# Optimization experiments

Measured on AMD Instinct MI355X. Metric: run time of the kernel, lower is better.

The kernel has to match this reference:

```python
import jax, jax.numpy as jnp
import numpy as np

N_NODES = 50000
N_EDGES = 800000
N_GRAPHS = 512
D = 128
NUM_LAYERS = 3
BN_EPS = 1e-5


def setup_inputs() -> dict:
    key = jax.random.key(0)
    ks = jax.random.split(key, 16)
    x = jax.random.normal(ks[0], (N_NODES, D), dtype=jnp.float32)
    edge_index = jax.random.randint(ks[1], (2, N_EDGES), 0, N_NODES, dtype=jnp.int64)
    batch = jnp.sort(jax.random.randint(ks[2], (N_NODES,), 0, N_GRAPHS, dtype=jnp.int64))
    # per-layer MLP params (all dims are 128 so we can stack across layers)
    s1 = 1.0 / np.sqrt(D)
    W1 = jax.random.uniform(ks[3], (NUM_LAYERS, D, D), jnp.float32, -s1, s1)
    b1 = jax.random.uniform(ks[4], (NUM_LAYERS, D), jnp.float32, -s1, s1)
    W2 = jax.random.uniform(ks[5], (NUM_LAYERS, D, D), jnp.float32, -s1, s1)
    b2 = jax.random.uniform(ks[6], (NUM_LAYERS, D), jnp.float32, -s1, s1)
    eps = jnp.zeros((NUM_LAYERS,), jnp.float32)  # train_eps=True, init 0.0
    gamma = jnp.ones((NUM_LAYERS, D), jnp.float32)
    beta = jnp.zeros((NUM_LAYERS, D), jnp.float32)
    return {"x": x, "edge_index": edge_index, "batch": batch,
            "W1": W1, "b1": b1, "W2": W2, "b2": b2,
            "eps": eps, "gamma": gamma, "beta": beta}


def _gin_forward(x, edge_index, batch, W1, b1, W2, b2, eps, gamma, beta):
    src, dst = edge_index[0], edge_index[1]
    h = x
    for i in range(NUM_LAYERS):
        # GINConv: MLP((1+eps)*h_i + sum_{j->i} h_j)  (scatter-add over edges)
        agg = jax.ops.segment_sum(h[src], dst, num_segments=N_NODES)
        z = (1.0 + eps[i]) * h + agg
        z = jax.nn.relu(z @ W1[i] + b1[i]) @ W2[i] + b2[i]
        # BatchNorm1d (training-mode batch stats, biased variance)
        mean = jnp.mean(z, axis=0)
        var = jnp.mean(jnp.square(z - mean), axis=0)
        h = (z - mean) * jax.lax.rsqrt(var + BN_EPS) * gamma[i] + beta[i]
        if i < NUM_LAYERS - 1:
            h = jax.nn.relu(h)  # dropout is identity in eval mode
    # global_mean_pool over batch segment ids
    sums = jax.ops.segment_sum(h, batch, num_segments=N_GRAPHS)
    counts = jax.ops.segment_sum(jnp.ones((N_NODES, 1), h.dtype), batch, num_segments=N_GRAPHS)
    return sums / jnp.maximum(counts, 1.0)


def reference(x, edge_index, batch, W1, b1, W2, b2, eps, gamma, beta):
    return _gin_forward(x, edge_index, batch, W1, b1, W2, b2, eps, gamma, beta)
```

## Files before the change

kernel.cpp:

```cpp
#include <hip/hip_runtime.h>

#define N_NODESC 50000
#define N_EDGESC 800000
#define N_GRAPHSC 512
#define DF 128
#define BN_EPSF 1e-5f
#define CSR_CAP 64
#define LAYER_BLOCKS 3125
#define NSLICE 32
#define POISON 0xAAAAAAAAu

#define PREP_SCAT_B 3125
#define PREP_CONVX_B 3125
#define PREP_CONVW_B 48
#define PREP_ZERO_B 6
#define PREP_TOTAL_B (PREP_SCAT_B + PREP_CONVX_B + PREP_CONVW_B + PREP_ZERO_B)

typedef _Float16 half8 __attribute__((ext_vector_type(8)));
typedef _Float16 half2v __attribute__((ext_vector_type(2)));
typedef float floatx4 __attribute__((ext_vector_type(4)));

__global__ __launch_bounds__(256) void k_prep(
    const int* __restrict__ src, const int* __restrict__ dst,
    unsigned* __restrict__ cursor, unsigned short* __restrict__ csr,
    const float* __restrict__ x, _Float16* __restrict__ h,
    const float* __restrict__ W1, const float* __restrict__ W2, half8* __restrict__ wf,
    float* __restrict__ pb2)
{
    int b = blockIdx.x;
    int tid = threadIdx.x;
    if (b < PREP_SCAT_B) {
        int e = b * 256 + tid;
        int d = dst[e];
        int sv = src[e];
        unsigned pos = atomicAdd(&cursor[d], 1u) - POISON;
        if (pos < CSR_CAP) csr[d * CSR_CAP + pos] = (unsigned short)sv;
    } else if (b < PREP_SCAT_B + PREP_CONVX_B) {
        int i8 = (b - PREP_SCAT_B) * 256 + tid;
        const floatx4* x4 = (const floatx4*)x;
        floatx4 v0 = __builtin_nontemporal_load(&x4[i8 * 2]);
        floatx4 v1 = __builtin_nontemporal_load(&x4[i8 * 2 + 1]);
        half8 o;
        o[0] = (_Float16)v0[0]; o[1] = (_Float16)v0[1]; o[2] = (_Float16)v0[2]; o[3] = (_Float16)v0[3];
        o[4] = (_Float16)v1[0]; o[5] = (_Float16)v1[1]; o[6] = (_Float16)v1[2]; o[7] = (_Float16)v1[3];
        ((half8*)h)[i8] = o;
    } else if (b < PREP_SCAT_B + PREP_CONVX_B + PREP_CONVW_B) {
        int t = (b - PREP_SCAT_B - PREP_CONVX_B) * 256 + tid;
        int m = t >> 11;
        int p = t & 2047;
        int ntile = p >> 8;
        int ks = (p >> 6) & 3;
        int l = p & 63;
        int n = ntile * 16 + (l & 15);
        int kb = ks * 32 + (l >> 4) * 8;
        const float* W = (m < 3) ? (W1 + (size_t)m * DF * DF) : (W2 + (size_t)(m - 3) * DF * DF);
        half8 o;
#pragma unroll
        for (int j = 0; j < 8; j++) o[j] = (_Float16)W[(size_t)(kb + j) * DF + n];
        wf[t] = o;
    } else {
        int b2 = b - (PREP_SCAT_B + PREP_CONVX_B + PREP_CONVW_B);
        floatx4* p4 = (floatx4*)pb2;
        int base = (b2 * 256 + tid) * 4;
#pragma unroll
        for (int j = 0; j < 4; j++) p4[base + j] = (floatx4)(0.f);
    }
}

#define TSTRIDE 136
template <int MODE>
__global__ __launch_bounds__(1024) void k_layer(
    const _Float16* __restrict__ Hin, const unsigned* __restrict__ cursor,
    const unsigned short* __restrict__ csr,
    const float* __restrict__ epsArr, int layer,
    const float* __restrict__ pbPrev, const float* __restrict__ gprev, const float* __restrict__ bprev,
    const half8* __restrict__ W1f, const float* __restrict__ b1,
    const half8* __restrict__ W2f, const float* __restrict__ b2,
    _Float16* __restrict__ Z, float* __restrict__ pbOut)
{
    __shared__ _Float16 At[16 * TSTRIDE];
    __shared__ _Float16 Bt[16 * TSTRIDE];
    __shared__ float red[4][256];
    __shared__ float scof[DF], ofof[DF];
    const int tid = threadIdx.x;
    const int w = tid >> 6, lane = tid & 63;

    if (MODE == 1) {
        int cc = tid & 255, sg = tid >> 8;
        float s = 0.f;
#pragma unroll
        for (int sl = 0; sl < 8; sl++) s += pbPrev[(sg + sl * 4) * 256 + cc];
        red[sg][cc] = s;
        __syncthreads();
        if (tid < 128) {
            const float invN = 1.f / (float)N_NODESC;
            float su = red[0][tid] + red[1][tid] + red[2][tid] + red[3][tid];
            float sq = red[0][128 + tid] + red[1][128 + tid] + red[2][128 + tid] + red[3][128 + tid];
            float m = su * invN;
            float var = sq * invN - m * m;
            float sc = gprev[tid] * rsqrtf(var + BN_EPSF);
            scof[tid] = sc;
            ofof[tid] = bprev[tid] - m * sc;
        }
        __syncthreads();
    }

    {
        int n = blockIdx.x * 16 + w;
        int g = lane >> 4, c16 = lane & 15;
        float sc[8], of[8];
        if (MODE == 1) {
#pragma unroll
            for (int i = 0; i < 8; i++) {
                sc[i] = scof[c16 * 8 + i];
                of[i] = ofof[c16 * 8 + i];
            }
        }
        const half8* Hr8 = (const half8*)Hin;
        int myidx = (int)csr[n * CSR_CAP + lane];
        int deg = (int)(cursor[n] - POISON);
        if (deg > CSR_CAP) deg = CSR_CAP;

        float a[8];
#pragma unroll
        for (int i = 0; i < 8; i++) a[i] = 0.f;
        if (g == 0) {
            half8 u = Hr8[(size_t)n * 16 + c16];
            float e1 = 1.0f + epsArr[layer];
#pragma unroll
            for (int i = 0; i < 8; i++) {
                float xv = (float)u[i];
                if (MODE == 1) xv = fmaxf(xv * sc[i] + of[i], 0.f);
                a[i] = e1 * xv;
            }
        }
        int T = (deg + 7) >> 3;
        int k = g;
        for (int t = 0; t < T; t++, k += 8) {
            int m0 = __shfl(myidx, k);
            int m1 = __shfl(myidx, k + 4);
            bool ok0 = k < deg, ok1 = (k + 4) < deg;
            int mm0 = ok0 ? m0 : n;
            int mm1 = ok1 ? m1 : n;
            half8 u0 = Hr8[(size_t)mm0 * 16 + c16];
            half8 u1 = Hr8[(size_t)mm1 * 16 + c16];
            float f0 = ok0 ? 1.f : 0.f, f1 = ok1 ? 1.f : 0.f;
#pragma unroll
            for (int i = 0; i < 8; i++) {
                float x0 = (float)u0[i], x1 = (float)u1[i];
                if (MODE == 1) {
                    x0 = fmaxf(x0 * sc[i] + of[i], 0.f);
                    x1 = fmaxf(x1 * sc[i] + of[i], 0.f);
                }
                a[i] = fmaf(f0, x0, a[i]);
                a[i] = fmaf(f1, x1, a[i]);
            }
        }
#pragma unroll
        for (int i = 0; i < 8; i++) {
            a[i] += __shfl_xor(a[i], 16);
            a[i] += __shfl_xor(a[i], 32);
        }
        if (g == 0) {
            half8 o;
#pragma unroll
            for (int i = 0; i < 8; i++) o[i] = (_Float16)a[i];
            *(half8*)&At[w * TSTRIDE + c16 * 8] = o;
        }
    }
    __syncthreads();

    const int q = lane >> 4, c = lane & 15;
    if (w < 8) {
        half8 af[4];
#pragma unroll
        for (int ks = 0; ks < 4; ks++)
            af[ks] = *(const half8*)&At[c * TSTRIDE + ks * 32 + q * 8];
        floatx4 acc = (floatx4)(0.0f);
#pragma unroll
        for (int ks = 0; ks < 4; ks++) {
            half8 wfr = W1f[(w * 4 + ks) * 64 + lane];
            acc = __builtin_amdgcn_mfma_f32_16x16x32_f16(af[ks], wfr, acc, 0, 0, 0);
        }
        float b = b1[w * 16 + c];
#pragma unroll
        for (int r = 0; r < 4; r++) {
            float vv = fmaxf(acc[r] + b, 0.f);
            Bt[(q * 4 + r) * TSTRIDE + w * 16 + c] = (_Float16)vv;
        }
    }
    __syncthreads();

    if (w < 8) {
        half8 bf[4];
#pragma unroll
        for (int ks = 0; ks < 4; ks++)
            bf[ks] = *(const half8*)&Bt[c * TSTRIDE + ks * 32 + q * 8];
        floatx4 acc2 = (floatx4)(0.0f);
#pragma unroll
        for (int ks = 0; ks < 4; ks++) {
            half8 wfr = W2f[(w * 4 + ks) * 64 + lane];
            acc2 = __builtin_amdgcn_mfma_f32_16x16x32_f16(bf[ks], wfr, acc2, 0, 0, 0);
        }
        float b = b2[w * 16 + c];
        float ls = 0.f, lq = 0.f;
#pragma unroll
        for (int r = 0; r < 4; r++) {
            float vv = acc2[r] + b;
            ls += vv;
            lq += vv * vv;
            At[(q * 4 + r) * TSTRIDE + w * 16 + c] = (_Float16)vv;
        }
        ls += __shfl_xor(ls, 16);
        ls += __shfl_xor(ls, 32);
        lq += __shfl_xor(lq, 16);
        lq += __shfl_xor(lq, 32);
        if (q == 0) {
            float* pbb = pbOut + (size_t)(blockIdx.x & (NSLICE - 1)) * 256;
            atomicAdd(&pbb[w * 16 + c], ls);
            atomicAdd(&pbb[128 + w * 16 + c], lq);
        }
    }
    __syncthreads();

    half2v vz = *(const half2v*)&At[w * TSTRIDE + 2 * lane];
    ((half2v*)Z)[(size_t)(blockIdx.x * 16 + w) * 64 + lane] = vz;
}

static __device__ int lbound(const int* __restrict__ a, int n, int key) {
    int lo = 0, hi = n;
    while (lo < hi) {
        int mid = (lo + hi) >> 1;
        if (a[mid] < key) lo = mid + 1; else hi = mid;
    }
    return lo;
}

__global__ __launch_bounds__(128) void k_pool(const _Float16* __restrict__ Z, const int* __restrict__ batch,
                                              const float* __restrict__ pbL2, const float* __restrict__ gamma,
                                              const float* __restrict__ beta, float* __restrict__ out) {
    __shared__ int bnds[2];
    int g = blockIdx.x, c = threadIdx.x;
    if (threadIdx.x == 0) {
        bnds[0] = lbound(batch, N_NODESC, g);
        bnds[1] = lbound(batch, N_NODESC, g + 1);
    }
    float su = 0.f, sq = 0.f;
#pragma unroll 8
    for (int sl = 0; sl < NSLICE; sl++) {
        su += pbL2[sl * 256 + c];
        sq += pbL2[sl * 256 + 128 + c];
    }
    __syncthreads();
    const float invN = 1.f / (float)N_NODESC;
    float m = su * invN;
    float v = sq * invN - m * m;
    float sc = gamma[c] * rsqrtf(v + BN_EPSF);
    float of = beta[c] - m * sc;
    int lo = bnds[0], hi = bnds[1];
    float s = 0.f;
    int r = lo;
    for (; r + 4 <= hi; r += 4) {
        s += (float)Z[(size_t)r * DF + c] + (float)Z[(size_t)(r + 1) * DF + c]
           + (float)Z[(size_t)(r + 2) * DF + c] + (float)Z[(size_t)(r + 3) * DF + c];
    }
    for (; r < hi; r++) s += (float)Z[(size_t)r * DF + c];
    int cnt = hi - lo;
    out[g * DF + c] = (cnt > 0) ? (s / (float)cnt) * sc + of : 0.f;
}

extern "C" void kernel_launch(void* const* d_in, const int* in_sizes, int n_in,
                              void* d_out, int out_size, void* d_ws, size_t ws_size,
                              hipStream_t stream) {
    const float* x     = (const float*)d_in[0];
    const int*   ei    = (const int*)d_in[1];
    const int*   batch = (const int*)d_in[2];
    const float* W1    = (const float*)d_in[3];
    const float* b1    = (const float*)d_in[4];
    const float* W2    = (const float*)d_in[5];
    const float* b2    = (const float*)d_in[6];
    const float* eps   = (const float*)d_in[7];
    const float* gamma = (const float*)d_in[8];
    const float* beta  = (const float*)d_in[9];
    float* out = (float*)d_out;

    char* ws = (char*)d_ws;
    size_t o = 0;
    auto alloc = [&](size_t bytes) -> char* {
        char* p = ws + o;
        o += (bytes + 255) & ~(size_t)255;
        return p;
    };
    unsigned* cursor = (unsigned*)alloc(N_NODESC * sizeof(unsigned));
    unsigned short* csr = (unsigned short*)alloc((size_t)N_NODESC * CSR_CAP * sizeof(unsigned short));
    float* pb2     = (float*)alloc((size_t)3 * NSLICE * 256 * sizeof(float));
    half8* wf      = (half8*)alloc((size_t)6 * 2048 * sizeof(half8));
    _Float16* hbuf = (_Float16*)alloc((size_t)N_NODESC * DF * sizeof(_Float16));
    _Float16* za   = (_Float16*)alloc((size_t)N_NODESC * DF * sizeof(_Float16));
    _Float16* zb   = (_Float16*)alloc((size_t)N_NODESC * DF * sizeof(_Float16));
    (void)ws_size; (void)in_sizes; (void)n_in; (void)out_size;

    const int* srcA = ei;
    const int* dstA = ei + N_EDGESC;

    k_prep<<<PREP_TOTAL_B, 256, 0, stream>>>(srcA, dstA, cursor, csr, x, hbuf, W1, W2, wf, pb2);

    k_layer<0><<<LAYER_BLOCKS, 1024, 0, stream>>>(
        hbuf, cursor, csr, eps, 0, nullptr, nullptr, nullptr,
        wf + 0 * 2048, b1 + 0 * DF, wf + 3 * 2048, b2 + 0 * DF, za, pb2 + 0 * 8192);
    k_layer<1><<<LAYER_BLOCKS, 1024, 0, stream>>>(
        za, cursor, csr, eps, 1, pb2 + 0 * 8192, gamma + 0 * DF, beta + 0 * DF,
        wf + 1 * 2048, b1 + 1 * DF, wf + 4 * 2048, b2 + 1 * DF, zb, pb2 + 1 * 8192);
    k_layer<1><<<LAYER_BLOCKS, 1024, 0, stream>>>(
        zb, cursor, csr, eps, 2, pb2 + 1 * 8192, gamma + 1 * DF, beta + 1 * DF,
        wf + 2 * 2048, b1 + 2 * DF, wf + 5 * 2048, b2 + 2 * DF, za, pb2 + 2 * 8192);
    k_pool<<<N_GRAPHSC, DF, 0, stream>>>(za, batch, pb2 + 2 * 8192, gamma + 2 * DF, beta + 2 * DF, out);
}
```

Measured before the change: 272.6 us.

## Fuse prep, three GIN layers and pooling into one cooperative persistent kernel

Replaces the five separate launches (prep, three layer kernels, pool) with a single cooperative kernel that strides over tiles and uses grid-wide syncs between phases. It aims to remove launch gaps and the tail of each kernel. In exchange the grid is capped at about two 1024-thread blocks per CU. Each grid.sync costs a global barrier, and the launch_bounds hint may raise register pressure and lower occupancy for the gather-bound layer work.

```diff
diff --git a/kernel.cpp b/kernel.cpp
--- a/kernel.cpp
+++ b/kernel.cpp
@@ -1,4 +1,7 @@
 #include <hip/hip_runtime.h>
+#include <hip/hip_cooperative_groups.h>
+
+namespace cg = cooperative_groups;
 
 #define N_NODESC 50000
 #define N_EDGESC 800000
@@ -14,218 +17,11 @@
 #define PREP_CONVX_B 3125
 #define PREP_CONVW_B 48
 #define PREP_ZERO_B 6
-#define PREP_TOTAL_B (PREP_SCAT_B + PREP_CONVX_B + PREP_CONVW_B + PREP_ZERO_B)
+#define PREP_UNITS (PREP_SCAT_B + PREP_CONVX_B + PREP_CONVW_B + PREP_ZERO_B)
 
 typedef _Float16 half8 __attribute__((ext_vector_type(8)));
 typedef _Float16 half2v __attribute__((ext_vector_type(2)));
 typedef float floatx4 __attribute__((ext_vector_type(4)));
-
-__global__ __launch_bounds__(256) void k_prep(
-    const int* __restrict__ src, const int* __restrict__ dst,
-    unsigned* __restrict__ cursor, unsigned short* __restrict__ csr,
-    const float* __restrict__ x, _Float16* __restrict__ h,
-    const float* __restrict__ W1, const float* __restrict__ W2, half8* __restrict__ wf,
-    float* __restrict__ pb2)
-{
-    int b = blockIdx.x;
-    int tid = threadIdx.x;
-    if (b < PREP_SCAT_B) {
-        int e = b * 256 + tid;
-        int d = dst[e];
-        int sv = src[e];
-        unsigned pos = atomicAdd(&cursor[d], 1u) - POISON;
-        if (pos < CSR_CAP) csr[d * CSR_CAP + pos] = (unsigned short)sv;
-    } else if (b < PREP_SCAT_B + PREP_CONVX_B) {
-        int i8 = (b - PREP_SCAT_B) * 256 + tid;
-        const floatx4* x4 = (const floatx4*)x;
-        floatx4 v0 = __builtin_nontemporal_load(&x4[i8 * 2]);
-        floatx4 v1 = __builtin_nontemporal_load(&x4[i8 * 2 + 1]);
-        half8 o;
-        o[0] = (_Float16)v0[0]; o[1] = (_Float16)v0[1]; o[2] = (_Float16)v0[2]; o[3] = (_Float16)v0[3];
-        o[4] = (_Float16)v1[0]; o[5] = (_Float16)v1[1]; o[6] = (_Float16)v1[2]; o[7] = (_Float16)v1[3];
-        ((half8*)h)[i8] = o;
-    } else if (b < PREP_SCAT_B + PREP_CONVX_B + PREP_CONVW_B) {
-        int t = (b - PREP_SCAT_B - PREP_CONVX_B) * 256 + tid;
-        int m = t >> 11;
-        int p = t & 2047;
-        int ntile = p >> 8;
-        int ks = (p >> 6) & 3;
-        int l = p & 63;
-        int n = ntile * 16 + (l & 15);
-        int kb = ks * 32 + (l >> 4) * 8;
-        const float* W = (m < 3) ? (W1 + (size_t)m * DF * DF) : (W2 + (size_t)(m - 3) * DF * DF);
-        half8 o;
-#pragma unroll
-        for (int j = 0; j < 8; j++) o[j] = (_Float16)W[(size_t)(kb + j) * DF + n];
-        wf[t] = o;
-    } else {
-        int b2 = b - (PREP_SCAT_B + PREP_CONVX_B + PREP_CONVW_B);
-        floatx4* p4 = (floatx4*)pb2;
-        int base = (b2 * 256 + tid) * 4;
-#pragma unroll
-        for (int j = 0; j < 4; j++) p4[base + j] = (floatx4)(0.f);
-    }
-}
-
-#define TSTRIDE 136
-template <int MODE>
-__global__ __launch_bounds__(1024) void k_layer(
-    const _Float16* __restrict__ Hin, const unsigned* __restrict__ cursor,
-    const unsigned short* __restrict__ csr,
-    const float* __restrict__ epsArr, int layer,
-    const float* __restrict__ pbPrev, const float* __restrict__ gprev, const float* __restrict__ bprev,
-    const half8* __restrict__ W1f, const float* __restrict__ b1,
-    const half8* __restrict__ W2f, const float* __restrict__ b2,
-    _Float16* __restrict__ Z, float* __restrict__ pbOut)
-{
-    __shared__ _Float16 At[16 * TSTRIDE];
-    __shared__ _Float16 Bt[16 * TSTRIDE];
-    __shared__ float red[4][256];
-    __shared__ float scof[DF], ofof[DF];
-    const int tid = threadIdx.x;
-    const int w = tid >> 6, lane = tid & 63;
-
-    if (MODE == 1) {
-        int cc = tid & 255, sg = tid >> 8;
-        float s = 0.f;
-#pragma unroll
-        for (int sl = 0; sl < 8; sl++) s += pbPrev[(sg + sl * 4) * 256 + cc];
-        red[sg][cc] = s;
-        __syncthreads();
-        if (tid < 128) {
-            const float invN = 1.f / (float)N_NODESC;
-            float su = red[0][tid] + red[1][tid] + red[2][tid] + red[3][tid];
-            float sq = red[0][128 + tid] + red[1][128 + tid] + red[2][128 + tid] + red[3][128 + tid];
-            float m = su * invN;
-            float var = sq * invN - m * m;
-            float sc = gprev[tid] * rsqrtf(var + BN_EPSF);
-            scof[tid] = sc;
-            ofof[tid] = bprev[tid] - m * sc;
-        }
-        __syncthreads();
-    }
-
-    {
-        int n = blockIdx.x * 16 + w;
-        int g = lane >> 4, c16 = lane & 15;
-        float sc[8], of[8];
-        if (MODE == 1) {
-#pragma unroll
-            for (int i = 0; i < 8; i++) {
-                sc[i] = scof[c16 * 8 + i];
-                of[i] = ofof[c16 * 8 + i];
-            }
-        }
-        const half8* Hr8 = (const half8*)Hin;
-        int myidx = (int)csr[n * CSR_CAP + lane];
-        int deg = (int)(cursor[n] - POISON);
-        if (deg > CSR_CAP) deg = CSR_CAP;
-
-        float a[8];
-#pragma unroll
-        for (int i = 0; i < 8; i++) a[i] = 0.f;
-        if (g == 0) {
-            half8 u = Hr8[(size_t)n * 16 + c16];
-            float e1 = 1.0f + epsArr[layer];
-#pragma unroll
-            for (int i = 0; i < 8; i++) {
-                float xv = (float)u[i];
-                if (MODE == 1) xv = fmaxf(xv * sc[i] + of[i], 0.f);
-                a[i] = e1 * xv;
-            }
-        }
-        int T = (deg + 7) >> 3;
-        int k = g;
-        for (int t = 0; t < T; t++, k += 8) {
-            int m0 = __shfl(myidx, k);
-            int m1 = __shfl(myidx, k + 4);
-            bool ok0 = k < deg, ok1 = (k + 4) < deg;
-            int mm0 = ok0 ? m0 : n;
-            int mm1 = ok1 ? m1 : n;
-            half8 u0 = Hr8[(size_t)mm0 * 16 + c16];
-            half8 u1 = Hr8[(size_t)mm1 * 16 + c16];
-            float f0 = ok0 ? 1.f : 0.f, f1 = ok1 ? 1.f : 0.f;
-#pragma unroll
-            for (int i = 0; i < 8; i++) {
-                float x0 = (float)u0[i], x1 = (float)u1[i];
-                if (MODE == 1) {
-                    x0 = fmaxf(x0 * sc[i] + of[i], 0.f);
-                    x1 = fmaxf(x1 * sc[i] + of[i], 0.f);
-                }
-                a[i] = fmaf(f0, x0, a[i]);
-                a[i] = fmaf(f1, x1, a[i]);
-            }
-        }
-#pragma unroll
-        for (int i = 0; i < 8; i++) {
-            a[i] += __shfl_xor(a[i], 16);
-            a[i] += __shfl_xor(a[i], 32);
-        }
-        if (g == 0) {
-            half8 o;
-#pragma unroll
-            for (int i = 0; i < 8; i++) o[i] = (_Float16)a[i];
-            *(half8*)&At[w * TSTRIDE + c16 * 8] = o;
-        }
-    }
-    __syncthreads();
-
-    const int q = lane >> 4, c = lane & 15;
-    if (w < 8) {
-        half8 af[4];
-#pragma unroll
-        for (int ks = 0; ks < 4; ks++)
-            af[ks] = *(const half8*)&At[c * TSTRIDE + ks * 32 + q * 8];
-        floatx4 acc = (floatx4)(0.0f);
-#pragma unroll
-        for (int ks = 0; ks < 4; ks++) {
-            half8 wfr = W1f[(w * 4 + ks) * 64 + lane];
-            acc = __builtin_amdgcn_mfma_f32_16x16x32_f16(af[ks], wfr, acc, 0, 0, 0);
-        }
-        float b = b1[w * 16 + c];
-#pragma unroll
-        for (int r = 0; r < 4; r++) {
-            float vv = fmaxf(acc[r] + b, 0.f);
-            Bt[(q * 4 + r) * TSTRIDE + w * 16 + c] = (_Float16)vv;
-        }
-    }
-    __syncthreads();
-
-    if (w < 8) {
-        half8 bf[4];
-#pragma unroll
-        for (int ks = 0; ks < 4; ks++)
-            bf[ks] = *(const half8*)&Bt[c * TSTRIDE + ks * 32 + q * 8];
-        floatx4 acc2 = (floatx4)(0.0f);
-#pragma unroll
-        for (int ks = 0; ks < 4; ks++) {
-            half8 wfr = W2f[(w * 4 + ks) * 64 + lane];
-            acc2 = __builtin_amdgcn_mfma_f32_16x16x32_f16(bf[ks], wfr, acc2, 0, 0, 0);
-        }
-        float b = b2[w * 16 + c];
-        float ls = 0.f, lq = 0.f;
-#pragma unroll
-        for (int r = 0; r < 4; r++) {
-            float vv = acc2[r] + b;
-            ls += vv;
-            lq += vv * vv;
-            At[(q * 4 + r) * TSTRIDE + w * 16 + c] = (_Float16)vv;
-        }
-        ls += __shfl_xor(ls, 16);
-        ls += __shfl_xor(ls, 32);
-        lq += __shfl_xor(lq, 16);
-        lq += __shfl_xor(lq, 32);
-        if (q == 0) {
-            float* pbb = pbOut + (size_t)(blockIdx.x & (NSLICE - 1)) * 256;
-            atomicAdd(&pbb[w * 16 + c], ls);
-            atomicAdd(&pbb[128 + w * 16 + c], lq);
-        }
-    }
-    __syncthreads();
-
-    half2v vz = *(const half2v*)&At[w * TSTRIDE + 2 * lane];
-    ((half2v*)Z)[(size_t)(blockIdx.x * 16 + w) * 64 + lane] = vz;
-}
 
 static __device__ int lbound(const int* __restrict__ a, int n, int key) {
     int lo = 0, hi = n;
@@ -236,37 +32,265 @@
     return lo;
 }
 
-__global__ __launch_bounds__(128) void k_pool(const _Float16* __restrict__ Z, const int* __restrict__ batch,
-                                              const float* __restrict__ pbL2, const float* __restrict__ gamma,
-                                              const float* __restrict__ beta, float* __restrict__ out) {
-    __shared__ int bnds[2];
-    int g = blockIdx.x, c = threadIdx.x;
-    if (threadIdx.x == 0) {
-        bnds[0] = lbound(batch, N_NODESC, g);
-        bnds[1] = lbound(batch, N_NODESC, g + 1);
+#define TSTRIDE 136
+
+__global__ __launch_bounds__(1024, 8) void k_all(
+    const int* __restrict__ src, const int* __restrict__ dst,
+    unsigned* __restrict__ cursor, unsigned short* __restrict__ csr,
+    const float* __restrict__ x, _Float16* __restrict__ hbuf,
+    const float* __restrict__ W1, const float* __restrict__ b1,
+    const float* __restrict__ W2, const float* __restrict__ b2,
+    half8* __restrict__ wf, float* __restrict__ pb2,
+    const float* __restrict__ epsArr, const float* __restrict__ gamma, const float* __restrict__ beta,
+    const int* __restrict__ batch, _Float16* __restrict__ za, _Float16* __restrict__ zb,
+    float* __restrict__ out)
+{
+    cg::grid_group grid = cg::this_grid();
+    const int tid = threadIdx.x;
+    const int nb = gridDim.x;
+
+    __shared__ _Float16 At[16 * TSTRIDE];
+    __shared__ _Float16 Bt[16 * TSTRIDE];
+    __shared__ float red[4][256];
+    __shared__ float scof[DF], ofof[DF];
+    __shared__ int bnds2[8][2];
+
+    for (int F = blockIdx.x * 1024 + tid; F < PREP_UNITS * 256; F += nb * 1024) {
+        int b = F >> 8;
+        int t2 = F & 255;
+        if (b < PREP_SCAT_B) {
+            int e = F;
+            int d = dst[e];
+            int sv = src[e];
+            unsigned pos = atomicAdd(&cursor[d], 1u) - POISON;
+            if (pos < CSR_CAP) csr[d * CSR_CAP + pos] = (unsigned short)sv;
+        } else if (b < PREP_SCAT_B + PREP_CONVX_B) {
+            int i8 = (b - PREP_SCAT_B) * 256 + t2;
+            const floatx4* x4 = (const floatx4*)x;
+            floatx4 v0 = __builtin_nontemporal_load(&x4[i8 * 2]);
+            floatx4 v1 = __builtin_nontemporal_load(&x4[i8 * 2 + 1]);
+            half8 o;
+            o[0] = (_Float16)v0[0]; o[1] = (_Float16)v0[1]; o[2] = (_Float16)v0[2]; o[3] = (_Float16)v0[3];
+            o[4] = (_Float16)v1[0]; o[5] = (_Float16)v1[1]; o[6] = (_Float16)v1[2]; o[7] = (_Float16)v1[3];
+            ((half8*)hbuf)[i8] = o;
+        } else if (b < PREP_SCAT_B + PREP_CONVX_B + PREP_CONVW_B) {
+            int t = (b - PREP_SCAT_B - PREP_CONVX_B) * 256 + t2;
+            int m = t >> 11;
+            int p = t & 2047;
+            int ntile = p >> 8;
+            int ks = (p >> 6) & 3;
+            int l = p & 63;
+            int n = ntile * 16 + (l & 15);
+            int kb = ks * 32 + (l >> 4) * 8;
+            const float* W = (m < 3) ? (W1 + (size_t)m * DF * DF) : (W2 + (size_t)(m - 3) * DF * DF);
+            half8 o;
+#pragma unroll
+            for (int j = 0; j < 8; j++) o[j] = (_Float16)W[(size_t)(kb + j) * DF + n];
+            wf[t] = o;
+        } else {
+            int b2 = b - (PREP_SCAT_B + PREP_CONVX_B + PREP_CONVW_B);
+            floatx4* p4 = (floatx4*)pb2;
+            int base = (b2 * 256 + t2) * 4;
+#pragma unroll
+            for (int j = 0; j < 4; j++) p4[base + j] = (floatx4)(0.f);
+        }
     }
-    float su = 0.f, sq = 0.f;
+    grid.sync();
+
+    const int w = tid >> 6, lane = tid & 63;
+    const int q = lane >> 4, c = lane & 15;
+
+    for (int l = 0; l < 3; l++) {
+        const _Float16* Hin = (l == 0) ? hbuf : ((l == 1) ? za : zb);
+        _Float16* Z = (l == 1) ? zb : za;
+        const half8* W1f = wf + (size_t)l * 2048;
+        const half8* W2f = wf + (size_t)(3 + l) * 2048;
+        const float* bb1 = b1 + l * DF;
+        const float* bb2 = b2 + l * DF;
+        float* pbOut = pb2 + (size_t)l * 8192;
+
+        if (l > 0) {
+            const float* pbPrev = pb2 + (size_t)(l - 1) * 8192;
+            const float* gprev = gamma + (l - 1) * DF;
+            const float* bprev = beta + (l - 1) * DF;
+            int cc = tid & 255, sg = tid >> 8;
+            float s = 0.f;
+#pragma unroll
+            for (int sl = 0; sl < 8; sl++) s += pbPrev[(sg + sl * 4) * 256 + cc];
+            red[sg][cc] = s;
+            __syncthreads();
+            if (tid < 128) {
+                const float invN = 1.f / (float)N_NODESC;
+                float su = red[0][tid] + red[1][tid] + red[2][tid] + red[3][tid];
+                float sq = red[0][128 + tid] + red[1][128 + tid] + red[2][128 + tid] + red[3][128 + tid];
+                float m = su * invN;
+                float var = sq * invN - m * m;
+                float sc = gprev[tid] * rsqrtf(var + BN_EPSF);
+                scof[tid] = sc;
+                ofof[tid] = bprev[tid] - m * sc;
+            }
+            __syncthreads();
+        }
+
+        const float e1 = 1.0f + epsArr[l];
+
+        for (int tile = blockIdx.x; tile < LAYER_BLOCKS; tile += nb) {
+            {
+                int n = tile * 16 + w;
+                int g = lane >> 4, c16 = lane & 15;
+                float sc[8], of[8];
+                if (l > 0) {
+#pragma unroll
+                    for (int i = 0; i < 8; i++) {
+                        sc[i] = scof[c16 * 8 + i];
+                        of[i] = ofof[c16 * 8 + i];
+                    }
+                }
+                const half8* Hr8 = (const half8*)Hin;
+                int myidx = (int)csr[n * CSR_CAP + lane];
+                int deg = (int)(cursor[n] - POISON);
+                if (deg > CSR_CAP) deg = CSR_CAP;
+
+                float a[8];
+#pragma unroll
+                for (int i = 0; i < 8; i++) a[i] = 0.f;
+                if (g == 0) {
+                    half8 u = Hr8[(size_t)n * 16 + c16];
+#pragma unroll
+                    for (int i = 0; i < 8; i++) {
+                        float xv = (float)u[i];
+                        if (l > 0) xv = fmaxf(xv * sc[i] + of[i], 0.f);
+                        a[i] = e1 * xv;
+                    }
+                }
+                int T = (deg + 7) >> 3;
+                int k = g;
+                for (int t = 0; t < T; t++, k += 8) {
+                    int m0 = __shfl(myidx, k);
+                    int m1 = __shfl(myidx, k + 4);
+                    bool ok0 = k < deg, ok1 = (k + 4) < deg;
+                    int mm0 = ok0 ? m0 : n;
+                    int mm1 = ok1 ? m1 : n;
+                    half8 u0 = Hr8[(size_t)mm0 * 16 + c16];
+                    half8 u1 = Hr8[(size_t)mm1 * 16 + c16];
+                    float f0 = ok0 ? 1.f : 0.f, f1 = ok1 ? 1.f : 0.f;
+#pragma unroll
+                    for (int i = 0; i < 8; i++) {
+                        float x0 = (float)u0[i], x1 = (float)u1[i];
+                        if (l > 0) {
+                            x0 = fmaxf(x0 * sc[i] + of[i], 0.f);
+                            x1 = fmaxf(x1 * sc[i] + of[i], 0.f);
+                        }
+                        a[i] = fmaf(f0, x0, a[i]);
+                        a[i] = fmaf(f1, x1, a[i]);
+                    }
+                }
+#pragma unroll
+                for (int i = 0; i < 8; i++) {
+                    a[i] += __shfl_xor(a[i], 16);
+                    a[i] += __shfl_xor(a[i], 32);
+                }
+                if (g == 0) {
+                    half8 o;
+#pragma unroll
+                    for (int i = 0; i < 8; i++) o[i] = (_Float16)a[i];
+                    *(half8*)&At[w * TSTRIDE + c16 * 8] = o;
+                }
+            }
+            __syncthreads();
+
+            if (w < 8) {
+                half8 af[4];
+#pragma unroll
+                for (int ks = 0; ks < 4; ks++)
+                    af[ks] = *(const half8*)&At[c * TSTRIDE + ks * 32 + q * 8];
+                floatx4 acc = (floatx4)(0.0f);
+#pragma unroll
+                for (int ks = 0; ks < 4; ks++) {
+                    half8 wfr = W1f[(w * 4 + ks) * 64 + lane];
+                    acc = __builtin_amdgcn_mfma_f32_16x16x32_f16(af[ks], wfr, acc, 0, 0, 0);
+                }
+                float b = bb1[w * 16 + c];
+#pragma unroll
+                for (int r = 0; r < 4; r++) {
+                    float vv = fmaxf(acc[r] + b, 0.f);
+                    Bt[(q * 4 + r) * TSTRIDE + w * 16 + c] = (_Float16)vv;
+                }
+            }
+            __syncthreads();
+
+            if (w < 8) {
+                half8 bf[4];
+#pragma unroll
+                for (int ks = 0; ks < 4; ks++)
+                    bf[ks] = *(const half8*)&Bt[c * TSTRIDE + ks * 32 + q * 8];
+                floatx4 acc2 = (floatx4)(0.0f);
+#pragma unroll
+                for (int ks = 0; ks < 4; ks++) {
+                    half8 wfr = W2f[(w * 4 + ks) * 64 + lane];
+                    acc2 = __builtin_amdgcn_mfma_f32_16x16x32_f16(bf[ks], wfr, acc2, 0, 0, 0);
+                }
+                float b = bb2[w * 16 + c];
+                float ls = 0.f, lq = 0.f;
+#pragma unroll
+                for (int r = 0; r < 4; r++) {
+                    float vv = acc2[r] + b;
+                    ls += vv;
+                    lq += vv * vv;
+                    At[(q * 4 + r) * TSTRIDE + w * 16 + c] = (_Float16)vv;
+                }
+                ls += __shfl_xor(ls, 16);
+                ls += __shfl_xor(ls, 32);
+                lq += __shfl_xor(lq, 16);
+                lq += __shfl_xor(lq, 32);
+                if (q == 0) {
+                    float* pbb = pbOut + (size_t)(tile & (NSLICE - 1)) * 256;
+                    atomicAdd(&pbb[w * 16 + c], ls);
+                    atomicAdd(&pbb[128 + w * 16 + c], lq);
+                }
+            }
+            __syncthreads();
+
+            half2v vz = *(const half2v*)&At[w * TSTRIDE + 2 * lane];
+            ((half2v*)Z)[(size_t)(tile * 16 + w) * 64 + lane] = vz;
+        }
+        grid.sync();
+    }
+
+    const float* pbL2 = pb2 + 2 * 8192;
+    const float* g2 = gamma + 2 * DF;
+    const float* be2 = beta + 2 * DF;
+    for (int gbase = blockIdx.x * 8; gbase < N_GRAPHSC; gbase += nb * 8) {
+        int j = tid >> 7;
+        int cc = tid & 127;
+        int g = gbase + j;
+        if (cc == 0) {
+            bnds2[j][0] = lbound(batch, N_NODESC, g);
+            bnds2[j][1] = lbound(batch, N_NODESC, g + 1);
+        }
+        float su = 0.f, sq = 0.f;
 #pragma unroll 8
-    for (int sl = 0; sl < NSLICE; sl++) {
-        su += pbL2[sl * 256 + c];
-        sq += pbL2[sl * 256 + 128 + c];
+        for (int sl = 0; sl < NSLICE; sl++) {
+            su += pbL2[sl * 256 + cc];
+            sq += pbL2[sl * 256 + 128 + cc];
+        }
+        __syncthreads();
+        const float invN = 1.f / (float)N_NODESC;
+        float m = su * invN;
+        float v = sq * invN - m * m;
+        float sc = g2[cc] * rsqrtf(v + BN_EPSF);
+        float of = be2[cc] - m * sc;
+        int lo = bnds2[j][0], hi = bnds2[j][1];
+        float s = 0.f;
+        int r = lo;
+        for (; r + 4 <= hi; r += 4) {
+            s += (float)za[(size_t)r * DF + cc] + (float)za[(size_t)(r + 1) * DF + cc]
+               + (float)za[(size_t)(r + 2) * DF + cc] + (float)za[(size_t)(r + 3) * DF + cc];
+        }
+        for (; r < hi; r++) s += (float)za[(size_t)r * DF + cc];
+        int cnt = hi - lo;
+        out[g * DF + cc] = (cnt > 0) ? (s / (float)cnt) * sc + of : 0.f;
     }
-    __syncthreads();
-    const float invN = 1.f / (float)N_NODESC;
-    float m = su * invN;
-    float v = sq * invN - m * m;
-    float sc = gamma[c] * rsqrtf(v + BN_EPSF);
-    float of = beta[c] - m * sc;
-    int lo = bnds[0], hi = bnds[1];
-    float s = 0.f;
-    int r = lo;
-    for (; r + 4 <= hi; r += 4) {
-        s += (float)Z[(size_t)r * DF + c] + (float)Z[(size_t)(r + 1) * DF + c]
-           + (float)Z[(size_t)(r + 2) * DF + c] + (float)Z[(size_t)(r + 3) * DF + c];
-    }
-    for (; r < hi; r++) s += (float)Z[(size_t)r * DF + c];
-    int cnt = hi - lo;
-    out[g * DF + c] = (cnt > 0) ? (s / (float)cnt) * sc + of : 0.f;
 }
 
 extern "C" void kernel_launch(void* const* d_in, const int* in_sizes, int n_in,
@@ -303,16 +327,18 @@
     const int* srcA = ei;
     const int* dstA = ei + N_EDGESC;
 
-    k_prep<<<PREP_TOTAL_B, 256, 0, stream>>>(srcA, dstA, cursor, csr, x, hbuf, W1, W2, wf, pb2);
-
-    k_layer<0><<<LAYER_BLOCKS, 1024, 0, stream>>>(
-        hbuf, cursor, csr, eps, 0, nullptr, nullptr, nullptr,
-        wf + 0 * 2048, b1 + 0 * DF, wf + 3 * 2048, b2 + 0 * DF, za, pb2 + 0 * 8192);
-    k_layer<1><<<LAYER_BLOCKS, 1024, 0, stream>>>(
-        za, cursor, csr, eps, 1, pb2 + 0 * 8192, gamma + 0 * DF, beta + 0 * DF,
-        wf + 1 * 2048, b1 + 1 * DF, wf + 4 * 2048, b2 + 1 * DF, zb, pb2 + 1 * 8192);
-    k_layer<1><<<LAYER_BLOCKS, 1024, 0, stream>>>(
-        zb, cursor, csr, eps, 2, pb2 + 1 * 8192, gamma + 1 * DF, beta + 1 * DF,
-        wf + 2 * 2048, b1 + 2 * DF, wf + 5 * 2048, b2 + 2 * DF, za, pb2 + 2 * 8192);
-    k_pool<<<N_GRAPHSC, DF, 0, stream>>>(za, batch, pb2 + 2 * 8192, gamma + 2 * DF, beta + 2 * DF, out);
+    int maxb = 0;
+    (void)hipOccupancyMaxActiveBlocksPerMultiprocessor(&maxb, k_all, 1024, 0);
+    int gridn = maxb * 256;
+    if (gridn > 512 || gridn <= 0) gridn = 512;
+
+    void* args[] = {
+        (void*)&srcA, (void*)&dstA, (void*)&cursor, (void*)&csr,
+        (void*)&x, (void*)&hbuf,
+        (void*)&W1, (void*)&b1, (void*)&W2, (void*)&b2,
+        (void*)&wf, (void*)&pb2,
+        (void*)&eps, (void*)&gamma, (void*)&beta,
+        (void*)&batch, (void*)&za, (void*)&zb, (void*)&out
+    };
+    hipLaunchCooperativeKernel((void*)k_all, dim3(gridn), dim3(1024), args, 0, stream);
 }
```

After: 579.2 us. 112% more time.
